# Kernel tuning notes

Hardware: AMD Instinct MI355X
Metric: run time of the kernel (lower is better)

The kernel has to match this reference:

```python
import jax, jax.numpy as jnp
import numpy as np


def setup_inputs() -> dict:
    key = jax.random.key(0)
    k1, k2, k3, k4, k5 = jax.random.split(key, 5)
    B, IN_N, POSE = 32, 8192, 64
    M = 8                     # matrix_pose_dim = sqrt(64)
    NH, S2, HID = 32, 256, 256  # in_n/(img^2), img^2, hidden_dim
    OUT_N = 64
    return {
        "current_pose": jax.random.normal(k1, (B, IN_N, POSE), jnp.float32),
        "w_current": 0.02 * jax.random.normal(k2, (1, 1, IN_N, M, M), jnp.float32),
        "w_next": 0.02 * jax.random.normal(k3, (OUT_N, M, M), jnp.float32),
        "E_proj": 0.02 * jax.random.normal(k4, (NH, S2, HID), jnp.float32),
        "rel_embedd": jax.random.normal(k5, (1, 1, POSE), jnp.float32),
    }


def reference(current_pose, w_current, w_next, E_proj, rel_embedd):
    B, IN_N, POSE = current_pose.shape
    M = w_current.shape[-1]           # matrix_pose_dim
    NH, S2, HID = E_proj.shape        # heads, img*img, hidden_dim
    OUT_N = w_next.shape[0]

    # w_current: (1,1,IN_N,M,M) -> (1,IN_N,M,M); per-capsule pose-matrix multiply
    wc = w_current.reshape(IN_N, M, M)[None]
    cp = current_pose.reshape(B, IN_N, M, M)
    cp = jnp.matmul(cp, wc)                      # (B, IN_N, M, M)

    # raw reshape (row-major, matches torch .reshape) then Linformer projection
    cp = cp.reshape(B, POSE, NH, 1, S2)
    cp = jnp.matmul(cp, E_proj)                  # (B, POSE, NH, 1, HID)
    cp = cp[:, :, :, 0, :]                       # squeeze(3) -> (B, POSE, NH, HID)
    cp = cp.reshape(B, NH * HID, POSE)           # raw reshape as in torch

    # dots = softmax over out_n axis of a constant tensor == uniform 1/OUT_N.
    # einsum('bij,bje->bie') with uniform dots == mean over j, broadcast over i.
    pooled = jnp.sum(cp, axis=1, keepdims=True) / OUT_N   # (B, 1, POSE)
    npc = jnp.broadcast_to(pooled, (B, OUT_N, POSE))

    # add relative embedding (h_out = w_out = output_img_size = 1)
    npc = npc.reshape(B, OUT_N, 1, 1, POSE) + rel_embedd  # (B,OUT_N,1,1,POSE)
    npc = jnp.transpose(npc, (0, 2, 3, 1, 4)).reshape(B, OUT_N, POSE)

    # next-layer pose-matrix multiply
    npc = npc.reshape(B, OUT_N, M, M)
    npc = jnp.matmul(npc, w_next[None])           # (B, OUT_N, M, M)
    npc = npc.reshape(B, 1, 1, OUT_N, POSE)
    return npc[:, 0]                              # squeeze(1) -> (B,1,OUT_N,POSE)
```

## Files before the change

kernel.cpp:

```cpp
#include <hip/hip_runtime.h>
#include <hip/hip_bf16.h>


typedef short short8_t __attribute__((ext_vector_type(8)));
typedef float f32x4_t __attribute__((ext_vector_type(4)));
typedef int   int4_t  __attribute__((ext_vector_type(4)));

__device__ __forceinline__ short f2bf(float f) {
    union { float f; unsigned u; } v; v.f = f;
    unsigned r = v.u + 0x7FFFu + ((v.u >> 16) & 1u);
    return (short)(r >> 16);
}

__device__ __forceinline__ int cvt_pk(float x, float y) {
    int r;
    asm("v_cvt_pk_bf16_f32 %0, %1, %2" : "=v"(r) : "v"(x), "v"(y));
    return r;
}

__global__ void k_prep(const float* __restrict__ WC, short* __restrict__ WCf,
                       const float* __restrict__ E, float* __restrict__ F) {
    if (blockIdx.x < 256) {
        int t   = blockIdx.x * 256 + threadIdx.x;
        int l   = t & 63;
        int pc  = (t >> 6) & 15;
        int rp  = t >> 10;
        int lhi = l >> 4;
        int j   = l & 15;
        int row = (pc * 4 + lhi) * 128 + rp * 2 + (j >> 3);
        const float* src = WC + ((size_t)row << 6) + (j & 7);
        short8_t o;
        #pragma unroll
        for (int k = 0; k < 8; ++k) o[k] = f2bf(src[k * 8]);
        ((short8_t*)WCf)[t] = o;
    } else {
        int idx = ((blockIdx.x - 256) * 256 + threadIdx.x) * 4;
        int q   = idx & 63;
        int row = idx >> 6;
        int r   = row >> 6;
        int e   = row & 63;
        int nh  = r >> 2;
        int s2  = ((r & 3) << 6) + e;
        const float* base = E + (((size_t)nh * 256 + s2) << 8) + q;
        float4 s0 = *(const float4*)(base);
        float4 s1 = *(const float4*)(base + 64);
        float4 s2v = *(const float4*)(base + 128);
        float4 s3 = *(const float4*)(base + 192);
        float4 o;
        o.x = s0.x + s1.x + s2v.x + s3.x;
        o.y = s0.y + s1.y + s2v.y + s3.y;
        o.z = s0.z + s1.z + s2v.z + s3.z;
        o.w = s0.w + s1.w + s2v.w + s3.w;
        *(float4*)(F + idx) = o;
    }
}

__global__ void k_bc(const float* __restrict__ CP, const short* __restrict__ WCf,
                     const float* __restrict__ F, float* __restrict__ P) {
    int b    = blockIdx.y;
    int gx   = blockIdx.x;
    int half = gx & 1;
    int rpg  = gx >> 1;
    int w = threadIdx.x >> 6;
    int l = threadIdx.x & 63;
    int rp = rpg * 4 + w;
    int r0 = rp * 2;

    int i16   = l & 15;
    int r_sel = i16 >> 3;
    int m1    = i16 & 7;
    int lhi   = l >> 4;

    __shared__ float Stile[512];
    __shared__ float red[4][64];

    const float* cp_base = CP + ((size_t)b << 19) + ((size_t)(r0 + r_sel) << 6) + m1 * 8;
    const short8_t* wf   = (const short8_t*)WCf + (size_t)rp * 1024 + (half * 8) * 64 + l;

    f32x4_t acc = {0.f, 0.f, 0.f, 0.f};
    #pragma unroll
    for (int c = 0; c < 8; ++c) {
        int p = (half * 8 + c) * 4 + lhi;
        const float* a_ptr = cp_base + ((size_t)p << 13);
        float4 a0 = *(const float4*)(a_ptr);
        float4 a1 = *(const float4*)(a_ptr + 4);
        int4_t ai;
        ai[0] = cvt_pk(a0.x, a0.y);
        ai[1] = cvt_pk(a0.z, a0.w);
        ai[2] = cvt_pk(a1.x, a1.y);
        ai[3] = cvt_pk(a1.z, a1.w);
        acc = __builtin_amdgcn_mfma_f32_16x16x32_bf16(
            __builtin_bit_cast(short8_t, ai), wf[c * 64], acc, 0, 0, 0);
    }
    int col = i16;
    #pragma unroll
    for (int v = 0; v < 4; ++v) {
        int row = lhi * 4 + v;
        if (row < 8 && col < 8)
            Stile[(w * 2 + 0) * 64 + row * 8 + col] = acc[v];
        else if (row >= 8 && col >= 8)
            Stile[(w * 2 + 1) * 64 + (row - 8) * 8 + (col - 8)] = acc[v];
    }
    __syncthreads();

    int q  = threadIdx.x & 63;
    int jg = threadIdx.x >> 6;
    const float* Fb = F + (((size_t)rpg * 512 + jg * 128) << 6) + q;
    const float* St = Stile + jg * 128;
    float p0 = 0.f, p1 = 0.f, p2 = 0.f, p3 = 0.f;
    #pragma unroll 8
    for (int s = 0; s < 128; s += 4) {
        p0 += St[s + 0] * Fb[(size_t)(s + 0) << 6];
        p1 += St[s + 1] * Fb[(size_t)(s + 1) << 6];
        p2 += St[s + 2] * Fb[(size_t)(s + 2) << 6];
        p3 += St[s + 3] * Fb[(size_t)(s + 3) << 6];
    }
    red[jg][q] = (p0 + p1) + (p2 + p3);
    __syncthreads();
    if (threadIdx.x < 64)
        P[((size_t)(b * 32 + gx) << 6) + threadIdx.x] =
            red[0][threadIdx.x] + red[1][threadIdx.x] +
            red[2][threadIdx.x] + red[3][threadIdx.x];
}

__global__ void k_final(const float* __restrict__ P, const float* __restrict__ rel,
                        const float* __restrict__ WN, float* __restrict__ out) {
    int b  = blockIdx.x;
    int oc = blockIdx.y;
    int t  = threadIdx.x;
    __shared__ float pool_s[64];
    if (t < 64) {
        float s = 0.f;
        #pragma unroll
        for (int c = 0; c < 32; ++c) s += P[((size_t)(b * 32 + c) << 6) + t];
        pool_s[t] = s * (1.0f / 64.0f) + rel[t];
    }
    __syncthreads();
    #pragma unroll
    for (int idx = t; idx < 1024; idx += 256) {
        int o = oc * 16 + (idx >> 6);
        int e = idx & 63;
        int m1 = e >> 3, m2 = e & 7;
        float a = 0.f;
        #pragma unroll
        for (int k = 0; k < 8; ++k)
            a += pool_s[m1 * 8 + k] * WN[o * 64 + k * 8 + m2];
        out[((size_t)b << 12) + o * 64 + e] = a;
    }
}

extern "C" void kernel_launch(void* const* d_in, const int* in_sizes, int n_in,
                              void* d_out, int out_size, void* d_ws, size_t ws_size,
                              hipStream_t stream) {
    const float* current_pose = (const float*)d_in[0];
    const float* w_current    = (const float*)d_in[1];
    const float* w_next       = (const float*)d_in[2];
    const float* E_proj       = (const float*)d_in[3];
    const float* rel_embedd   = (const float*)d_in[4];
    float* out = (float*)d_out;

    char* ws = (char*)d_ws;
    float* F   = (float*)(ws);
    short* WCf = (short*)(ws + (2u << 20));
    float* P   = (float*)(ws + (3u << 20));

    k_prep<<<dim3(768), dim3(256), 0, stream>>>(w_current, WCf, E_proj, F);
    k_bc<<<dim3(32, 32), dim3(256), 0, stream>>>(current_pose, WCf, F, P);
    k_final<<<dim3(32, 4), dim3(256), 0, stream>>>(P, rel_embedd, w_next, out);
}
```

Before: 29.21 us.

## Split k_bc into quarters, vectorize projection and reduce partials in final kernel

Each k_bc block now covers a quarter of the pose-matrix chunks, which doubles the grid to 64x32 blocks. The F projection uses float4 loads with wave shuffles instead of a shared-memory reduction plus a second barrier. Each wave writes its own partial, and k_final now sums 256 partials per batch with one block per batch. This raises parallelism and cuts barriers in k_bc, at the cost of more partial traffic and a heavier k_final running on fewer blocks.

Result: slower. 34.38 us (+17.7%).

```diff
diff --git a/kernel.cpp b/kernel.cpp
--- a/kernel.cpp
+++ b/kernel.cpp
@@ -59,8 +59,8 @@
                      const float* __restrict__ F, float* __restrict__ P) {
     int b    = blockIdx.y;
     int gx   = blockIdx.x;
-    int half = gx & 1;
-    int rpg  = gx >> 1;
+    int quarter = gx & 3;
+    int rpg  = gx >> 2;
     int w = threadIdx.x >> 6;
     int l = threadIdx.x & 63;
     int rp = rpg * 4 + w;
@@ -72,15 +72,14 @@
     int lhi   = l >> 4;
 
     __shared__ float Stile[512];
-    __shared__ float red[4][64];
 
     const float* cp_base = CP + ((size_t)b << 19) + ((size_t)(r0 + r_sel) << 6) + m1 * 8;
-    const short8_t* wf   = (const short8_t*)WCf + (size_t)rp * 1024 + (half * 8) * 64 + l;
+    const short8_t* wf   = (const short8_t*)WCf + (size_t)rp * 1024 + (quarter * 4) * 64 + l;
 
     f32x4_t acc = {0.f, 0.f, 0.f, 0.f};
     #pragma unroll
-    for (int c = 0; c < 8; ++c) {
-        int p = (half * 8 + c) * 4 + lhi;
+    for (int c = 0; c < 4; ++c) {
+        int p = (quarter * 4 + c) * 4 + lhi;
         const float* a_ptr = cp_base + ((size_t)p << 13);
         float4 a0 = *(const float4*)(a_ptr);
         float4 a1 = *(const float4*)(a_ptr + 4);
@@ -103,49 +102,61 @@
     }
     __syncthreads();
 
-    int q  = threadIdx.x & 63;
-    int jg = threadIdx.x >> 6;
-    const float* Fb = F + (((size_t)rpg * 512 + jg * 128) << 6) + q;
-    const float* St = Stile + jg * 128;
-    float p0 = 0.f, p1 = 0.f, p2 = 0.f, p3 = 0.f;
+    int g  = l >> 4;
+    int ql = l & 15;
+    const float* Fb = F + (((size_t)rpg * 512 + w * 128 + g) << 6) + ql * 4;
+    const float* St = Stile + w * 128 + g;
+    f32x4_t pacc = {0.f, 0.f, 0.f, 0.f};
     #pragma unroll 8
-    for (int s = 0; s < 128; s += 4) {
-        p0 += St[s + 0] * Fb[(size_t)(s + 0) << 6];
-        p1 += St[s + 1] * Fb[(size_t)(s + 1) << 6];
-        p2 += St[s + 2] * Fb[(size_t)(s + 2) << 6];
-        p3 += St[s + 3] * Fb[(size_t)(s + 3) << 6];
+    for (int s = 0; s < 32; ++s) {
+        float sv = St[s * 4];
+        float4 fv = *(const float4*)(Fb + ((size_t)(s * 4) << 6));
+        pacc[0] += sv * fv.x;
+        pacc[1] += sv * fv.y;
+        pacc[2] += sv * fv.z;
+        pacc[3] += sv * fv.w;
     }
-    red[jg][q] = (p0 + p1) + (p2 + p3);
-    __syncthreads();
-    if (threadIdx.x < 64)
-        P[((size_t)(b * 32 + gx) << 6) + threadIdx.x] =
-            red[0][threadIdx.x] + red[1][threadIdx.x] +
-            red[2][threadIdx.x] + red[3][threadIdx.x];
+    #pragma unroll
+    for (int c = 0; c < 4; ++c) {
+        pacc[c] += __shfl_xor(pacc[c], 16, 64);
+        pacc[c] += __shfl_xor(pacc[c], 32, 64);
+    }
+    if (l < 16) {
+        float4 o; o.x = pacc[0]; o.y = pacc[1]; o.z = pacc[2]; o.w = pacc[3];
+        *(float4*)(P + ((size_t)((b * 64 + gx) * 4 + w) << 6) + ql * 4) = o;
+    }
 }
 
 __global__ void k_final(const float* __restrict__ P, const float* __restrict__ rel,
                         const float* __restrict__ WN, float* __restrict__ out) {
     int b  = blockIdx.x;
-    int oc = blockIdx.y;
     int t  = threadIdx.x;
+    int q    = t & 63;
+    int sgrp = t >> 6;
+    const float* Pb = P + ((size_t)b << 14);
+    float s = 0.f;
+    #pragma unroll 8
+    for (int c = sgrp * 64; c < sgrp * 64 + 64; ++c)
+        s += Pb[((size_t)c << 6) + q];
+    __shared__ float red[4][64];
+    red[sgrp][q] = s;
+    __syncthreads();
     __shared__ float pool_s[64];
     if (t < 64) {
-        float s = 0.f;
-        #pragma unroll
-        for (int c = 0; c < 32; ++c) s += P[((size_t)(b * 32 + c) << 6) + t];
-        pool_s[t] = s * (1.0f / 64.0f) + rel[t];
+        pool_s[t] = (red[0][t] + red[1][t] + red[2][t] + red[3][t]) * (1.0f / 64.0f)
+                    + rel[t];
     }
     __syncthreads();
     #pragma unroll
-    for (int idx = t; idx < 1024; idx += 256) {
-        int o = oc * 16 + (idx >> 6);
+    for (int idx = t; idx < 4096; idx += 256) {
+        int o = idx >> 6;
         int e = idx & 63;
         int m1 = e >> 3, m2 = e & 7;
         float a = 0.f;
         #pragma unroll
         for (int k = 0; k < 8; ++k)
             a += pool_s[m1 * 8 + k] * WN[o * 64 + k * 8 + m2];
-        out[((size_t)b << 12) + o * 64 + e] = a;
+        out[((size_t)b << 12) + idx] = a;
     }
 }
 
@@ -165,6 +176,6 @@
     float* P   = (float*)(ws + (3u << 20));
 
     k_prep<<<dim3(768), dim3(256), 0, stream>>>(w_current, WCf, E_proj, F);
-    k_bc<<<dim3(32, 32), dim3(256), 0, stream>>>(current_pose, WCf, F, P);
-    k_final<<<dim3(32, 4), dim3(256), 0, stream>>>(P, rel_embedd, w_next, out);
+    k_bc<<<dim3(64, 32), dim3(256), 0, stream>>>(current_pose, WCf, F, P);
+    k_final<<<dim3(32), dim3(256), 0, stream>>>(P, rel_embedd, w_next, out);
 }
```
